# Performance work log

Hardware: AMD Instinct MI355X
Metric: run time of the kernel (lower is better)

Reference implementation:

```python
import jax, jax.numpy as jnp
import numpy as np

HID = (128, 256, 128)  # nmp_qc NNet hidden layer sizes
D_IN = 256
TARGET = 256


def _mlp_params(key, n_in, n_out, prefix):
    sizes = (n_in,) + HID + (n_out,)
    params = {}
    for i in range(len(sizes) - 1):
        key, k1, k2 = jax.random.split(key, 3)
        fan_in = sizes[i]
        bound = 1.0 / np.sqrt(fan_in)
        params[f"{prefix}_W{i}"] = jax.random.uniform(k1, (sizes[i], sizes[i + 1]), jnp.float32, -bound, bound)
        params[f"{prefix}_b{i}"] = jax.random.uniform(k2, (sizes[i + 1],), jnp.float32, -bound, bound)
    return params, key


def _mlp(x, Ws, bs):
    # ReLU on all layers except the last (linear output), matching NNet
    for i in range(len(Ws) - 1):
        x = jax.nn.relu(x @ Ws[i] + bs[i])
    return x @ Ws[-1] + bs[-1]


def setup_inputs() -> dict:
    key = jax.random.key(0)
    k0, k1, key = jax.random.split(key, 3)
    B, N = 512, 256
    inp = {
        "h0": jax.random.normal(k0, (B, N, D_IN), jnp.float32),
        "hT": jax.random.normal(k1, (B, N, D_IN), jnp.float32),
    }
    gp, key = _mlp_params(key, 2 * D_IN, TARGET, "g")  # gate MLP: concat(h0,hT) -> target
    op, key = _mlp_params(key, D_IN, TARGET, "o")      # value MLP: hT -> target
    inp.update(gp)
    inp.update(op)
    return inp


def reference(h0, hT,
              g_W0, g_b0, g_W1, g_b1, g_W2, g_b2, g_W3, g_b3,
              o_W0, o_b0, o_W1, o_b1, o_W2, o_b2, o_W3, o_b3):
    gWs = (g_W0, g_W1, g_W2, g_W3)
    gbs = (g_b0, g_b1, g_b2, g_b3)
    oWs = (o_W0, o_W1, o_W2, o_W3)
    obs = (o_b0, o_b1, o_b2, o_b3)
    # gate: sigmoid(MLP1([h0; hT])) ; value: MLP2(hT)  -- all [B, N, target]
    gate = jax.nn.sigmoid(_mlp(jnp.concatenate([h0, hT], axis=-1), gWs, gbs))
    val = _mlp(hT, oWs, obs)
    # node validity mask: sum of initial features > 0, matching r_mpnn
    mask = (jnp.sum(h0, axis=-1, keepdims=True) > 0).astype(h0.dtype)  # [B, N, 1]
    return jnp.sum(mask * gate * val, axis=1)  # [B, target]
```

## Files before the change

kernel.cpp:

```cpp
#include <hip/hip_runtime.h>
#include <hip/hip_bf16.h>
#include <stdint.h>


typedef __attribute__((ext_vector_type(8))) short short8_t;
typedef __attribute__((ext_vector_type(16))) float f32x16;

#define ROWS 64
#define NWG  2048
#define NTHR 256

#define OFF_P     0
#define OFF_A     17408
#define OFF_MASK  34816
#define LDS_TOTAL 35072

__device__ __forceinline__ short f2bf(float f) {
  union { float f; uint32_t u; } v; v.f = f;
  uint32_t r = (v.u + 0x7FFFu + ((v.u >> 16) & 1u)) >> 16;
  return (short)r;
}
__device__ __forceinline__ float bf2f(short b) {
  union { uint32_t u; float f; } v; v.u = ((uint32_t)(uint16_t)b) << 16;
  return v.f;
}

template <int KT16, int KSTEPS>
__device__ __forceinline__ void gemm32(const short* actin, int Sin,
                                       const short* __restrict__ wsB, int ks0, int cb,
                                       f32x16 (&acc)[2], int lane) {
  const int n32 = lane & 31, q32 = lane >> 5;
#pragma unroll
  for (int ks = 0; ks < KSTEPS; ++ks) {
    const int kl = ks * 16 + q32 * 8;
    const short8_t b = *(const short8_t*)(wsB + ((cb * KT16 + ks0 + ks) << 9) + lane * 8);
    short8_t a[2];
#pragma unroll
    for (int rt = 0; rt < 2; ++rt)
      a[rt] = *(const short8_t*)(actin + (rt * 32 + n32) * Sin + kl);
#pragma unroll
    for (int rt = 0; rt < 2; ++rt)
      acc[rt] = __builtin_amdgcn_mfma_f32_32x32x16_bf16(a[rt], b, acc[rt], 0, 0, 0);
  }
}

template <int ACTF>
__device__ __forceinline__ void epi32(f32x16 (&acc)[2], short* actout, int Sout,
                                      const float* __restrict__ bias, int c0,
                                      int n32, int q32) {
  const int c = c0 + n32;
  const float bv = bias[c];
#pragma unroll
  for (int rt = 0; rt < 2; ++rt)
#pragma unroll
    for (int reg = 0; reg < 16; ++reg) {
      const int r = rt * 32 + (reg & 3) + 8 * (reg >> 2) + 4 * q32;
      float v = acc[rt][reg] + bv;
      if (ACTF == 1) v = fmaxf(v, 0.f);
      actout[r * Sout + c] = f2bf(v);
    }
}

__device__ __forceinline__ void stage_half(const float* __restrict__ src, int row0,
                                           int colbase, int rowoff, short* Pb,
                                           float* maskacc, int mmode, int tid) {
  const int c4 = tid & 31, rb = tid >> 5;
  float4 v[4];
#pragma unroll
  for (int it = 0; it < 4; ++it)
    v[it] = *(const float4*)(src + (size_t)(row0 + rowoff + rb + it * 8) * 256 + colbase + c4 * 4);
#pragma unroll
  for (int it = 0; it < 4; ++it) {
    const int r = rowoff + rb + it * 8;
    short4 pk; pk.x = f2bf(v[it].x); pk.y = f2bf(v[it].y); pk.z = f2bf(v[it].z); pk.w = f2bf(v[it].w);
    *(short4*)(Pb + r * 136 + c4 * 4) = pk;
    if (mmode) {
      float s = v[it].x + v[it].y + v[it].z + v[it].w;
      s += __shfl_down(s, 16, 32);
      s += __shfl_down(s, 8, 32);
      s += __shfl_down(s, 4, 32);
      s += __shfl_down(s, 2, 32);
      s += __shfl_down(s, 1, 32);
      if (c4 == 0) {
        if (mmode == 1) maskacc[r] = s; else maskacc[r] += s;
      }
    }
  }
}

template <int NCH, bool MASKA>
__device__ __forceinline__ void stream32(const float* __restrict__ src0,
                                         const float* __restrict__ src1, int splitc,
                                         const short* __restrict__ wsB,
                                         const float* __restrict__ bias,
                                         short* P, short* A, float* maskacc,
                                         int row0, int tid, int wq, int lane) {
  constexpr int KT16 = NCH * 8;
  const int n32 = lane & 31, q32 = lane >> 5;
  f32x16 acc[2];
  acc[0] = (f32x16)(0.f); acc[1] = (f32x16)(0.f);
#pragma unroll
  for (int kc = 0; kc < NCH; ++kc) {
    const bool lo = (kc < splitc);
    const float* src = lo ? src0 : src1;
    const int colbase = (lo ? kc : kc - splitc) * 128;
    const int mm = MASKA ? (kc == 0 ? 1 : (lo ? 2 : 0)) : 0;
    stage_half(src, row0, colbase, 0,  P, maskacc, mm, tid);
    stage_half(src, row0, colbase, 32, P, maskacc, mm, tid);
    __syncthreads();
    gemm32<KT16, 8>(P, 136, wsB, kc * 8, wq, acc, lane);
    __syncthreads();
  }
  epi32<1>(acc, A, 136, bias, wq * 32, n32, q32);
  __syncthreads();
}

__device__ __forceinline__ void mid_pair(short* A, short* P,
                                         const short* __restrict__ ws1,
                                         const float* __restrict__ b1,
                                         const short* __restrict__ ws2,
                                         const float* __restrict__ b2,
                                         int wq, int lane) {
  const int n32 = lane & 31, q32 = lane >> 5;
  f32x16 acc2[2];
  acc2[0] = (f32x16)(0.f); acc2[1] = (f32x16)(0.f);
#pragma unroll
  for (int h = 0; h < 2; ++h) {
    f32x16 acc1[2];
    acc1[0] = (f32x16)(0.f); acc1[1] = (f32x16)(0.f);
    gemm32<8, 8>(A, 136, ws1, 0, h * 4 + wq, acc1, lane);
    epi32<1>(acc1, P, 136, b1 + h * 128, wq * 32, n32, q32);
    __syncthreads();
    gemm32<16, 8>(P, 136, ws2, h * 8, wq, acc2, lane);
    __syncthreads();
  }
  epi32<1>(acc2, A, 136, b2, wq * 32, n32, q32);
  __syncthreads();
}

__device__ __forceinline__ void gate_layer(const short* A, const short* __restrict__ wsB,
                                           const float* __restrict__ bias,
                                           uint32_t (&gate)[2][2][8],
                                           int wq, int lane) {
  const int n32 = lane & 31;
#pragma unroll
  for (int h = 0; h < 2; ++h) {
    f32x16 acc[2];
    acc[0] = (f32x16)(0.f); acc[1] = (f32x16)(0.f);
    gemm32<8, 8>(A, 136, wsB, 0, h * 4 + wq, acc, lane);
    const float bv = bias[h * 128 + wq * 32 + n32];
#pragma unroll
    for (int rt = 0; rt < 2; ++rt)
#pragma unroll
      for (int p = 0; p < 8; ++p) {
        const float g0 = 1.f / (1.f + __expf(-(acc[rt][2 * p] + bv)));
        const float g1 = 1.f / (1.f + __expf(-(acc[rt][2 * p + 1] + bv)));
        gate[rt][h][p] = ((uint32_t)(uint16_t)f2bf(g1) << 16) | (uint32_t)(uint16_t)f2bf(g0);
      }
  }
}

__device__ __forceinline__ void final32(const short* A, const short* __restrict__ wsB,
                                        const float* __restrict__ bias,
                                        const uint32_t (&gate)[2][2][8],
                                        const float* maskacc, float* __restrict__ out,
                                        int row0, int wq, int lane) {
  const int n32 = lane & 31, q32 = lane >> 5;
  const int b = row0 >> 8;
#pragma unroll
  for (int h = 0; h < 2; ++h) {
    f32x16 acc[2];
    acc[0] = (f32x16)(0.f); acc[1] = (f32x16)(0.f);
    gemm32<8, 8>(A, 136, wsB, 0, h * 4 + wq, acc, lane);
    const int c = h * 128 + wq * 32 + n32;
    const float bv = bias[c];
    float s = 0.f;
#pragma unroll
    for (int rt = 0; rt < 2; ++rt)
#pragma unroll
      for (int p = 0; p < 8; ++p) {
        const int r0 = rt * 32 + ((2 * p) & 3) + 8 * (p >> 1) + 4 * q32;
        const float g0 = bf2f((short)(gate[rt][h][p] & 0xFFFF));
        const float g1 = bf2f((short)(gate[rt][h][p] >> 16));
        const float v0 = acc[rt][2 * p] + bv;
        const float v1 = acc[rt][2 * p + 1] + bv;
        if (maskacc[r0] > 0.f)     s += g0 * v0;
        if (maskacc[r0 + 1] > 0.f) s += g1 * v1;
      }
    s += __shfl_down(s, 32);
    if (lane < 32) atomicAdd(out + b * 256 + c, s);
  }
}

__global__ __launch_bounds__(NTHR, 4)
void readout_main(const float* __restrict__ h0, const float* __restrict__ hT,
                  const short* __restrict__ ws,
                  const float* __restrict__ gb0, const float* __restrict__ gb1,
                  const float* __restrict__ gb2, const float* __restrict__ gb3,
                  const float* __restrict__ ob0, const float* __restrict__ ob1,
                  const float* __restrict__ ob2, const float* __restrict__ ob3,
                  float* __restrict__ out) {
  __shared__ __align__(16) char smem[LDS_TOTAL];
  short* P  = (short*)(smem + OFF_P);
  short* A  = (short*)(smem + OFF_A);
  float* maskacc = (float*)(smem + OFF_MASK);

  const int tid = threadIdx.x, lane = tid & 63, wq = tid >> 6;
  const int row0 = blockIdx.x * ROWS;
  uint32_t gate[2][2][8];

  stream32<4, true>(h0, hT, 2, ws + 0, gb0, P, A, maskacc, row0, tid, wq, lane);
  mid_pair(A, P, ws + 65536, gb1, ws + 98304, gb2, wq, lane);
  gate_layer(A, ws + 131072, gb3, gate, wq, lane);
  stream32<2, false>(hT, hT, 2, ws + 163840, ob0, P, A, maskacc, row0, tid, wq, lane);
  mid_pair(A, P, ws + 196608, ob1, ws + 229376, ob2, wq, lane);
  final32(A, ws + 262144, ob3, gate, maskacc, out, row0, wq, lane);
}

__global__ void prep(const float* __restrict__ W0, const float* __restrict__ W1,
                     const float* __restrict__ W2, const float* __restrict__ W3,
                     const float* __restrict__ W4, const float* __restrict__ W5,
                     const float* __restrict__ W6, const float* __restrict__ W7,
                     short* __restrict__ ws, float* __restrict__ out) {
  const int l = blockIdx.y;
  const int le = blockIdx.x * 256 + threadIdx.x;
  if (l == 1) { out[le] = 0.f; out[le + 65536] = 0.f; }
  int K, N, off; const float* W;
  switch (l) {
    case 0:  K = 512; N = 128; off = 0;      W = W0; break;
    case 1:  K = 128; N = 256; off = 65536;  W = W1; break;
    case 2:  K = 256; N = 128; off = 98304;  W = W2; break;
    case 3:  K = 128; N = 256; off = 131072; W = W3; break;
    case 4:  K = 256; N = 128; off = 163840; W = W4; break;
    case 5:  K = 128; N = 256; off = 196608; W = W5; break;
    case 6:  K = 256; N = 128; off = 229376; W = W6; break;
    default: K = 128; N = 256; off = 262144; W = W7; break;
  }
  if (le >= K * N) return;
  const int j = le & 7;
  const int lanei = (le >> 3) & 63;
  const int blk = le >> 9;
  const int kt16 = K >> 4;
  const int ks = blk % kt16, cb = blk / kt16;
  const int n = cb * 32 + (lanei & 31);
  const int k = ks * 16 + (lanei >> 5) * 8 + j;
  ws[off + le] = f2bf(W[k * N + n]);
}

extern "C" void kernel_launch(void* const* d_in, const int* in_sizes, int n_in,
                              void* d_out, int out_size, void* d_ws, size_t ws_size,
                              hipStream_t stream) {
  const float* h0  = (const float*)d_in[0];
  const float* hT  = (const float*)d_in[1];
  const float* gW0 = (const float*)d_in[2];  const float* gb0 = (const float*)d_in[3];
  const float* gW1 = (const float*)d_in[4];  const float* gb1 = (const float*)d_in[5];
  const float* gW2 = (const float*)d_in[6];  const float* gb2 = (const float*)d_in[7];
  const float* gW3 = (const float*)d_in[8];  const float* gb3 = (const float*)d_in[9];
  const float* oW0 = (const float*)d_in[10]; const float* ob0 = (const float*)d_in[11];
  const float* oW1 = (const float*)d_in[12]; const float* ob1 = (const float*)d_in[13];
  const float* oW2 = (const float*)d_in[14]; const float* ob2 = (const float*)d_in[15];
  const float* oW3 = (const float*)d_in[16]; const float* ob3 = (const float*)d_in[17];
  float* out = (float*)d_out;
  short* ws  = (short*)d_ws;

  prep<<<dim3(256, 8), 256, 0, stream>>>(gW0, gW1, gW2, gW3, oW0, oW1, oW2, oW3, ws, out);
  readout_main<<<NWG, NTHR, 0, stream>>>(h0, hT, ws,
                                         gb0, gb1, gb2, gb3,
                                         ob0, ob1, ob2, ob3, out);
}
```

Baseline: 450.9 us.

## Restructure readout into single-wave 32-row blocks and fuse final gate/value layers

Switches from 4-wave workgroups on 64 rows to single-wave workgroups of 32 rows, where each wave computes all output columns. This removes every __syncthreads between staging and the GEMM layers. The sigmoid gate layer is deferred and fused with the value MLP's last layer, so gate values no longer sit packed in registers across the value branch. LDS buffers shrink and are re-laid out into X/Y/Z regions. The cost is that each wave now streams the full weight set for every 32 rows, roughly doubling weight reads from cache, and each wave issues longer dependent load/MFMA sequences with fewer waves to hide latency.

```diff
diff --git a/kernel.cpp b/kernel.cpp
--- a/kernel.cpp
+++ b/kernel.cpp
@@ -6,75 +6,74 @@
 typedef __attribute__((ext_vector_type(8))) short short8_t;
 typedef __attribute__((ext_vector_type(16))) float f32x16;
 
-#define ROWS 64
-#define NWG  2048
-#define NTHR 256
-
-#define OFF_P     0
-#define OFF_A     17408
-#define OFF_MASK  34816
-#define LDS_TOTAL 35072
+#define ROWS 32
+#define NWG  4096
+#define NTHR 64
+
+#define OFF_X 0
+#define OFF_Y 8704
+#define OFF_Z 17408
+#define OFF_M 22016
+#define LDS_TOTAL 22144
 
 __device__ __forceinline__ short f2bf(float f) {
   union { float f; uint32_t u; } v; v.f = f;
   uint32_t r = (v.u + 0x7FFFu + ((v.u >> 16) & 1u)) >> 16;
   return (short)r;
 }
-__device__ __forceinline__ float bf2f(short b) {
-  union { uint32_t u; float f; } v; v.u = ((uint32_t)(uint16_t)b) << 16;
-  return v.f;
-}
-
-template <int KT16, int KSTEPS>
-__device__ __forceinline__ void gemm32(const short* actin, int Sin,
-                                       const short* __restrict__ wsB, int ks0, int cb,
-                                       f32x16 (&acc)[2], int lane) {
+
+template <int KT16, int KSTEPS, int CT>
+__device__ __forceinline__ void gemmW(const short* actin, int Sin,
+                                      const short* __restrict__ wsB, int ks0, int cb0,
+                                      f32x16 (&acc)[CT], int lane) {
   const int n32 = lane & 31, q32 = lane >> 5;
 #pragma unroll
   for (int ks = 0; ks < KSTEPS; ++ks) {
     const int kl = ks * 16 + q32 * 8;
-    const short8_t b = *(const short8_t*)(wsB + ((cb * KT16 + ks0 + ks) << 9) + lane * 8);
-    short8_t a[2];
-#pragma unroll
-    for (int rt = 0; rt < 2; ++rt)
-      a[rt] = *(const short8_t*)(actin + (rt * 32 + n32) * Sin + kl);
-#pragma unroll
-    for (int rt = 0; rt < 2; ++rt)
-      acc[rt] = __builtin_amdgcn_mfma_f32_32x32x16_bf16(a[rt], b, acc[rt], 0, 0, 0);
-  }
-}
-
-template <int ACTF>
-__device__ __forceinline__ void epi32(f32x16 (&acc)[2], short* actout, int Sout,
-                                      const float* __restrict__ bias, int c0,
-                                      int n32, int q32) {
-  const int c = c0 + n32;
-  const float bv = bias[c];
-#pragma unroll
-  for (int rt = 0; rt < 2; ++rt)
+    short8_t b[CT];
+#pragma unroll
+    for (int ct = 0; ct < CT; ++ct)
+      b[ct] = *(const short8_t*)(wsB + (((cb0 + ct) * KT16 + ks0 + ks) << 9) + lane * 8);
+    const short8_t a = *(const short8_t*)(actin + n32 * Sin + kl);
+#pragma unroll
+    for (int ct = 0; ct < CT; ++ct)
+      acc[ct] = __builtin_amdgcn_mfma_f32_32x32x16_bf16(a, b[ct], acc[ct], 0, 0, 0);
+  }
+}
+
+template <int CT, int ACTF>
+__device__ __forceinline__ void epiW(f32x16 (&acc)[CT], short* actout, int Sout,
+                                     const float* __restrict__ bias, int c0,
+                                     int n32, int q32) {
+#pragma unroll
+  for (int ct = 0; ct < CT; ++ct) {
+    const int c = c0 + ct * 32 + n32;
+    const float bv = bias[c0 + ct * 32 + n32];
 #pragma unroll
     for (int reg = 0; reg < 16; ++reg) {
-      const int r = rt * 32 + (reg & 3) + 8 * (reg >> 2) + 4 * q32;
-      float v = acc[rt][reg] + bv;
+      const int r = (reg & 3) + 8 * (reg >> 2) + 4 * q32;
+      float v = acc[ct][reg] + bv;
       if (ACTF == 1) v = fmaxf(v, 0.f);
       actout[r * Sout + c] = f2bf(v);
     }
-}
-
-__device__ __forceinline__ void stage_half(const float* __restrict__ src, int row0,
-                                           int colbase, int rowoff, short* Pb,
-                                           float* maskacc, int mmode, int tid) {
-  const int c4 = tid & 31, rb = tid >> 5;
-  float4 v[4];
-#pragma unroll
-  for (int it = 0; it < 4; ++it)
-    v[it] = *(const float4*)(src + (size_t)(row0 + rowoff + rb + it * 8) * 256 + colbase + c4 * 4);
-#pragma unroll
-  for (int it = 0; it < 4; ++it) {
-    const int r = rowoff + rb + it * 8;
+  }
+}
+
+template <bool MASKA>
+__device__ __forceinline__ void stage_chunk(const float* __restrict__ src, int row0,
+                                            int colbase, short* X, float* maskacc,
+                                            int mmode, int lane) {
+  const int c4 = lane & 31, rh = lane >> 5;
+  float4 v[16];
+#pragma unroll
+  for (int it = 0; it < 16; ++it)
+    v[it] = *(const float4*)(src + (size_t)(row0 + 2 * it + rh) * 256 + colbase + c4 * 4);
+#pragma unroll
+  for (int it = 0; it < 16; ++it) {
+    const int r = 2 * it + rh;
     short4 pk; pk.x = f2bf(v[it].x); pk.y = f2bf(v[it].y); pk.z = f2bf(v[it].z); pk.w = f2bf(v[it].w);
-    *(short4*)(Pb + r * 136 + c4 * 4) = pk;
-    if (mmode) {
+    *(short4*)(X + r * 136 + c4 * 4) = pk;
+    if (MASKA && mmode) {
       float s = v[it].x + v[it].y + v[it].z + v[it].w;
       s += __shfl_down(s, 16, 32);
       s += __shfl_down(s, 8, 32);
@@ -89,110 +88,84 @@
 }
 
 template <int NCH, bool MASKA>
-__device__ __forceinline__ void stream32(const float* __restrict__ src0,
-                                         const float* __restrict__ src1, int splitc,
-                                         const short* __restrict__ wsB,
-                                         const float* __restrict__ bias,
-                                         short* P, short* A, float* maskacc,
-                                         int row0, int tid, int wq, int lane) {
+__device__ __forceinline__ void streamW(const float* __restrict__ src0,
+                                        const float* __restrict__ src1, int splitc,
+                                        const short* __restrict__ wsB,
+                                        const float* __restrict__ bias,
+                                        short* X, short* Aout, float* maskacc,
+                                        int row0, int lane) {
   constexpr int KT16 = NCH * 8;
   const int n32 = lane & 31, q32 = lane >> 5;
-  f32x16 acc[2];
-  acc[0] = (f32x16)(0.f); acc[1] = (f32x16)(0.f);
+  f32x16 acc[4];
+#pragma unroll
+  for (int ct = 0; ct < 4; ++ct) acc[ct] = (f32x16)(0.f);
 #pragma unroll
   for (int kc = 0; kc < NCH; ++kc) {
     const bool lo = (kc < splitc);
     const float* src = lo ? src0 : src1;
     const int colbase = (lo ? kc : kc - splitc) * 128;
     const int mm = MASKA ? (kc == 0 ? 1 : (lo ? 2 : 0)) : 0;
-    stage_half(src, row0, colbase, 0,  P, maskacc, mm, tid);
-    stage_half(src, row0, colbase, 32, P, maskacc, mm, tid);
-    __syncthreads();
-    gemm32<KT16, 8>(P, 136, wsB, kc * 8, wq, acc, lane);
-    __syncthreads();
-  }
-  epi32<1>(acc, A, 136, bias, wq * 32, n32, q32);
-  __syncthreads();
-}
-
-__device__ __forceinline__ void mid_pair(short* A, short* P,
+    stage_chunk<MASKA>(src, row0, colbase, X, maskacc, mm, lane);
+    gemmW<KT16, 8, 4>(X, 136, wsB, kc * 8, 0, acc, lane);
+  }
+  epiW<4, 1>(acc, Aout, 136, bias, 0, n32, q32);
+}
+
+__device__ __forceinline__ void mid_pair(short* A, short* Z,
                                          const short* __restrict__ ws1,
                                          const float* __restrict__ b1,
                                          const short* __restrict__ ws2,
                                          const float* __restrict__ b2,
-                                         int wq, int lane) {
-  const int n32 = lane & 31, q32 = lane >> 5;
-  f32x16 acc2[2];
-  acc2[0] = (f32x16)(0.f); acc2[1] = (f32x16)(0.f);
-#pragma unroll
-  for (int h = 0; h < 2; ++h) {
+                                         int lane) {
+  const int n32 = lane & 31, q32 = lane >> 5;
+  f32x16 acc2[4];
+#pragma unroll
+  for (int ct = 0; ct < 4; ++ct) acc2[ct] = (f32x16)(0.f);
+#pragma unroll
+  for (int q = 0; q < 4; ++q) {
     f32x16 acc1[2];
     acc1[0] = (f32x16)(0.f); acc1[1] = (f32x16)(0.f);
-    gemm32<8, 8>(A, 136, ws1, 0, h * 4 + wq, acc1, lane);
-    epi32<1>(acc1, P, 136, b1 + h * 128, wq * 32, n32, q32);
-    __syncthreads();
-    gemm32<16, 8>(P, 136, ws2, h * 8, wq, acc2, lane);
-    __syncthreads();
-  }
-  epi32<1>(acc2, A, 136, b2, wq * 32, n32, q32);
-  __syncthreads();
-}
-
-__device__ __forceinline__ void gate_layer(const short* A, const short* __restrict__ wsB,
-                                           const float* __restrict__ bias,
-                                           uint32_t (&gate)[2][2][8],
-                                           int wq, int lane) {
-  const int n32 = lane & 31;
-#pragma unroll
-  for (int h = 0; h < 2; ++h) {
-    f32x16 acc[2];
-    acc[0] = (f32x16)(0.f); acc[1] = (f32x16)(0.f);
-    gemm32<8, 8>(A, 136, wsB, 0, h * 4 + wq, acc, lane);
-    const float bv = bias[h * 128 + wq * 32 + n32];
-#pragma unroll
-    for (int rt = 0; rt < 2; ++rt)
-#pragma unroll
-      for (int p = 0; p < 8; ++p) {
-        const float g0 = 1.f / (1.f + __expf(-(acc[rt][2 * p] + bv)));
-        const float g1 = 1.f / (1.f + __expf(-(acc[rt][2 * p + 1] + bv)));
-        gate[rt][h][p] = ((uint32_t)(uint16_t)f2bf(g1) << 16) | (uint32_t)(uint16_t)f2bf(g0);
+    gemmW<8, 8, 2>(A, 136, ws1, 0, q * 2, acc1, lane);
+    epiW<2, 1>(acc1, Z, 72, b1 + q * 64, 0, n32, q32);
+    gemmW<16, 4, 4>(Z, 72, ws2, q * 4, 0, acc2, lane);
+  }
+  epiW<4, 1>(acc2, A, 136, b2, 0, n32, q32);
+}
+
+__device__ __forceinline__ void final_fuse(const short* Ag, const short* Av,
+                                           const short* __restrict__ wsg,
+                                           const float* __restrict__ bg,
+                                           const short* __restrict__ wsv,
+                                           const float* __restrict__ bv,
+                                           const float* maskacc, float* __restrict__ out,
+                                           int bidx, int lane) {
+  const int n32 = lane & 31, q32 = lane >> 5;
+#pragma unroll
+  for (int q = 0; q < 4; ++q) {
+    f32x16 ag[2]; ag[0] = (f32x16)(0.f); ag[1] = (f32x16)(0.f);
+    gemmW<8, 8, 2>(Ag, 136, wsg, 0, q * 2, ag, lane);
+    f32x16 av[2]; av[0] = (f32x16)(0.f); av[1] = (f32x16)(0.f);
+    gemmW<8, 8, 2>(Av, 136, wsv, 0, q * 2, av, lane);
+#pragma unroll
+    for (int ct = 0; ct < 2; ++ct) {
+      const int c = q * 64 + ct * 32 + n32;
+      const float gb = bg[c], ob = bv[c];
+      float s = 0.f;
+#pragma unroll
+      for (int reg = 0; reg < 16; ++reg) {
+        const int r = (reg & 3) + 8 * (reg >> 2) + 4 * q32;
+        if (maskacc[r] > 0.f) {
+          const float g = 1.f / (1.f + __expf(-(ag[ct][reg] + gb)));
+          s += g * (av[ct][reg] + ob);
+        }
       }
-  }
-}
-
-__device__ __forceinline__ void final32(const short* A, const short* __restrict__ wsB,
-                                        const float* __restrict__ bias,
-                                        const uint32_t (&gate)[2][2][8],
-                                        const float* maskacc, float* __restrict__ out,
-                                        int row0, int wq, int lane) {
-  const int n32 = lane & 31, q32 = lane >> 5;
-  const int b = row0 >> 8;
-#pragma unroll
-  for (int h = 0; h < 2; ++h) {
-    f32x16 acc[2];
-    acc[0] = (f32x16)(0.f); acc[1] = (f32x16)(0.f);
-    gemm32<8, 8>(A, 136, wsB, 0, h * 4 + wq, acc, lane);
-    const int c = h * 128 + wq * 32 + n32;
-    const float bv = bias[c];
-    float s = 0.f;
-#pragma unroll
-    for (int rt = 0; rt < 2; ++rt)
-#pragma unroll
-      for (int p = 0; p < 8; ++p) {
-        const int r0 = rt * 32 + ((2 * p) & 3) + 8 * (p >> 1) + 4 * q32;
-        const float g0 = bf2f((short)(gate[rt][h][p] & 0xFFFF));
-        const float g1 = bf2f((short)(gate[rt][h][p] >> 16));
-        const float v0 = acc[rt][2 * p] + bv;
-        const float v1 = acc[rt][2 * p + 1] + bv;
-        if (maskacc[r0] > 0.f)     s += g0 * v0;
-        if (maskacc[r0 + 1] > 0.f) s += g1 * v1;
-      }
-    s += __shfl_down(s, 32);
-    if (lane < 32) atomicAdd(out + b * 256 + c, s);
-  }
-}
-
-__global__ __launch_bounds__(NTHR, 4)
+      s += __shfl_down(s, 32);
+      if (lane < 32) atomicAdd(out + bidx * 256 + c, s);
+    }
+  }
+}
+
+__global__ __launch_bounds__(NTHR, 2)
 void readout_main(const float* __restrict__ h0, const float* __restrict__ hT,
                   const short* __restrict__ ws,
                   const float* __restrict__ gb0, const float* __restrict__ gb1,
@@ -201,20 +174,20 @@
                   const float* __restrict__ ob2, const float* __restrict__ ob3,
                   float* __restrict__ out) {
   __shared__ __align__(16) char smem[LDS_TOTAL];
-  short* P  = (short*)(smem + OFF_P);
-  short* A  = (short*)(smem + OFF_A);
-  float* maskacc = (float*)(smem + OFF_MASK);
-
-  const int tid = threadIdx.x, lane = tid & 63, wq = tid >> 6;
+  short* X = (short*)(smem + OFF_X);
+  short* Y = (short*)(smem + OFF_Y);
+  short* Z = (short*)(smem + OFF_Z);
+  float* maskacc = (float*)(smem + OFF_M);
+
+  const int lane = threadIdx.x;
   const int row0 = blockIdx.x * ROWS;
-  uint32_t gate[2][2][8];
-
-  stream32<4, true>(h0, hT, 2, ws + 0, gb0, P, A, maskacc, row0, tid, wq, lane);
-  mid_pair(A, P, ws + 65536, gb1, ws + 98304, gb2, wq, lane);
-  gate_layer(A, ws + 131072, gb3, gate, wq, lane);
-  stream32<2, false>(hT, hT, 2, ws + 163840, ob0, P, A, maskacc, row0, tid, wq, lane);
-  mid_pair(A, P, ws + 196608, ob1, ws + 229376, ob2, wq, lane);
-  final32(A, ws + 262144, ob3, gate, maskacc, out, row0, wq, lane);
+  const int bidx = row0 >> 8;
+
+  streamW<4, true>(h0, hT, 2, ws + 0, gb0, X, Y, maskacc, row0, lane);
+  mid_pair(Y, Z, ws + 65536, gb1, ws + 98304, gb2, lane);
+  streamW<2, false>(hT, hT, 2, ws + 163840, ob0, X, X, maskacc, row0, lane);
+  mid_pair(X, Z, ws + 196608, ob1, ws + 229376, ob2, lane);
+  final_fuse(Y, X, ws + 131072, gb3, ws + 262144, ob3, maskacc, out, bidx, lane);
 }
 
 __global__ void prep(const float* __restrict__ W0, const float* __restrict__ W1,
```

Result: slower. 523.9 us (+16.2%).
